# Performance work log

Hardware: AMD Instinct MI355X
Metric: run time of the kernel (lower is better)

The kernel has to match this reference:

```python
import jax, jax.numpy as jnp
import numpy as np

K = 2048          # codes per class
NC = 8            # num_classes
CD = 256          # conv_dims
SP = 4            # latent spatial (28 -> 14 -> 7 -> 4)
D = CD * SP * SP  # 4096 codebook vector dim
N = 512           # RoIs


def _conv(x, W, b, stride, pad):
    y = jax.lax.conv_general_dilated(x, W, (stride, stride), [(pad, pad), (pad, pad)],
                                     dimension_numbers=('NCHW', 'OIHW', 'NCHW'))
    return y + b[None, :, None, None]


def _upsample2_ac(x):
    # bilinear upsample x2 with align_corners=True (torch nn.Upsample semantics)
    n, ch, H, W = x.shape
    Ho, Wo = 2 * H, 2 * W
    ys = jnp.arange(Ho) * (H - 1) / (Ho - 1)
    xs = jnp.arange(Wo) * (W - 1) / (Wo - 1)
    y0 = jnp.floor(ys).astype(jnp.int32); y1 = jnp.minimum(y0 + 1, H - 1)
    x0 = jnp.floor(xs).astype(jnp.int32); x1 = jnp.minimum(x0 + 1, W - 1)
    wy = (ys - y0).astype(x.dtype); wx = (xs - x0).astype(x.dtype)
    r = x[:, :, y0, :] * (1 - wy)[None, None, :, None] + x[:, :, y1, :] * wy[None, None, :, None]
    return r[:, :, :, x0] * (1 - wx)[None, None, None, :] + r[:, :, :, x1] * wx[None, None, None, :]


def setup_inputs() -> dict:
    key = jax.random.key(0)
    ks = jax.random.split(key, 20)
    s = 0.02
    inp = {
        'x': jax.random.normal(ks[0], (N, 1, 28, 28), jnp.float32),
        'We0': jax.random.normal(ks[1], (CD, 1, 3, 3), jnp.float32) * s,
        'be0': jnp.zeros((CD,), jnp.float32),
        'We1': jax.random.normal(ks[2], (CD, CD, 3, 3), jnp.float32) * s,
        'be1': jnp.zeros((CD,), jnp.float32),
        'We2': jax.random.normal(ks[3], (CD, CD, 3, 3), jnp.float32) * s,
        'be2': jnp.zeros((CD,), jnp.float32),
        'E': jax.random.normal(ks[4], (K * NC, D), jnp.float32) * s,
        'Wd0': jax.random.normal(ks[5], (CD, CD, 3, 3), jnp.float32) * s,
        'bd0': jnp.zeros((CD,), jnp.float32),
        'Wd1': jax.random.normal(ks[6], (CD, CD, 3, 3), jnp.float32) * s,
        'bd1': jnp.zeros((CD,), jnp.float32),
        'Wd2': jax.random.normal(ks[7], (CD, CD, 3, 3), jnp.float32) * s,
        'bd2': jnp.zeros((CD,), jnp.float32),
        'Wo': jax.random.normal(ks[8], (1, CD, 3, 3), jnp.float32) * s,
        'bo': jnp.zeros((1,), jnp.float32),
        'c': jax.random.randint(ks[9], (N,), 0, NC, jnp.int32),
    }
    return inp


def reference(x, We0, be0, We1, be1, We2, be2, E, Wd0, bd0, Wd1, bd1, Wd2, bd2, Wo, bo, c):
    # ---- encoder: 3 stride-2 convs, relu on all but the last ----
    h = jax.nn.relu(_conv(x, We0, be0, 2, 1))   # [N,CD,14,14]
    h = jax.nn.relu(_conv(h, We1, be1, 2, 1))   # [N,CD,7,7]
    h = _conv(h, We2, be2, 2, 1)                # [N,CD,4,4]
    z_e = h.reshape(N, D)                       # flattened latent, == z_e_x [N,D,1,1]

    # ---- class-conditional VQ ----
    # torch code loops over unique classes and concatenates -> output is in
    # stable-sorted-by-class order; replicate via stable argsort permutation.
    perm = jnp.argsort(c)  # stable
    # distances to the FULL table, then mask codes outside the sample's class slice
    d2 = (jnp.sum(z_e * z_e, axis=1, keepdims=True)         # [N,1]
          - 2.0 * z_e @ E.T                                  # [N,K*NC]
          + jnp.sum(E * E, axis=1)[None, :])
    code_cls = jnp.arange(K * NC, dtype=c.dtype) // K        # class of each code row
    d2 = jnp.where(code_cls[None, :] == c[:, None], d2, jnp.inf)
    idx = jnp.argmin(d2, axis=1)                             # global code index (includes key*K offset)

    q_det = jax.lax.stop_gradient(E)[idx]                    # vq_st uses detached codebook
    z_q_st = z_e + jax.lax.stop_gradient(q_det - z_e)        # straight-through
    z_q_bar = E[idx]                                         # gradient flows to codebook

    z_q_st_p = z_q_st[perm]
    z_q_bar_p = z_q_bar[perm]

    # ---- decoder: (upsample2 bilinear ac + conv + relu) x3, pad=0 on layer k==num_conv-2 ----
    xd = z_q_st_p.reshape(N, CD, SP, SP)
    xd = jax.nn.relu(_conv(_upsample2_ac(xd), Wd0, bd0, 1, 1))  # 4->8
    xd = jax.nn.relu(_conv(_upsample2_ac(xd), Wd1, bd1, 1, 0))  # 8->16->14
    xd = jax.nn.relu(_conv(_upsample2_ac(xd), Wd2, bd2, 1, 1))  # 14->28
    x_tilde = jax.nn.sigmoid(_conv(xd, Wo, bo, 1, 1))           # [N,1,28,28]

    return (x_tilde, z_e.reshape(N, D, 1, 1), z_q_bar_p.reshape(N, D, 1, 1))
```

## Files before the change

kernel.cpp:

```cpp
#include <hip/hip_runtime.h>
#include <hip/hip_bf16.h>
#include <cstdint>
#include <cstddef>

#define CDIV(a,b) (((a)+(b)-1)/(b))

typedef __attribute__((ext_vector_type(8))) short vbf8;
typedef __attribute__((ext_vector_type(4))) float vf4;

__device__ inline unsigned short f2bf(float f) {
  unsigned u = __float_as_uint(f);
  unsigned r = (u + 0x7fffu + ((u >> 16) & 1u)) >> 16;
  return (unsigned short)r;
}
__device__ inline float bf2f(unsigned short h) { return __uint_as_float(((unsigned)h) << 16); }

__global__ __launch_bounds__(256) void conv_e0_cl_kernel(
    const float* __restrict__ x, const float* __restrict__ W,
    const float* __restrict__ b, unsigned short* __restrict__ hi,
    unsigned short* __restrict__ lo)
{
  __shared__ float s_img[784];
  const int n = blockIdx.x;
  const int co = threadIdx.x;
  for (int i = threadIdx.x; i < 784; i += 256) s_img[i] = x[(size_t)n*784 + i];
  float w[9];
#pragma unroll
  for (int t = 0; t < 9; ++t) w[t] = W[co*9 + t];
  const float bb = b[co];
  __syncthreads();
  for (int p = 0; p < 196; ++p) {
    int y = p / 14, xo = p % 14;
    float a = bb;
#pragma unroll
    for (int t = 0; t < 9; ++t) {
      int yi = 2*y + t/3 - 1, xi = 2*xo + t%3 - 1;
      if (yi >= 0 && yi < 28 && xi >= 0 && xi < 28) a = fmaf(w[t], s_img[yi*28 + xi], a);
    }
    a = fmaxf(a, 0.f);
    unsigned short h = f2bf(a);
    size_t oidx = ((size_t)n*196 + p)*256 + co;
    hi[oidx] = h;
    lo[oidx] = f2bf(a - bf2f(h));
  }
}

__global__ __launch_bounds__(256) void wprep2_kernel(
    const float* __restrict__ W, unsigned short* __restrict__ Whi,
    unsigned short* __restrict__ Wlo)
{
  int idx = blockIdx.x*256 + threadIdx.x;
  if (idx >= 589824) return;
  int j   = idx & 7;
  int co  = (idx >> 3) & 255;
  int cig = (idx >> 11) & 31;
  int t   = idx >> 16;
  int ci  = cig*8 + j;
  float w = W[((size_t)co*256 + ci)*9 + t];
  unsigned short h = f2bf(w);
  Whi[idx] = h;
  Wlo[idx] = f2bf(w - bf2f(h));
}

template<int STRIDE, int HO, int WO, int WOP, int ROWS, int HI, int WI, int PAD,
         int ACT, int SPLIT, int OUTMODE>
__global__ __launch_bounds__(256, 2) void convmfma_kernel(
    const unsigned short* __restrict__ inT, const unsigned short* __restrict__ inTlo,
    const vbf8* __restrict__ Wt, const vbf8* __restrict__ Wtlo,
    const float* __restrict__ bias,
    unsigned short* __restrict__ outT, unsigned short* __restrict__ outTlo,
    float* __restrict__ outF)
{
  constexpr int NFM = ROWS*WOP/16;
  constexpr int RIN = (ROWS-1)*STRIDE + 3;
  constexpr int WS  = (WOP-1)*STRIDE + 3;
  constexpr int NG  = SPLIT ? 12 : 4;
  __shared__ vbf8 sA[RIN*WS*8];

  const int n  = blockIdx.x;
  const int y0 = blockIdx.y * ROWS;
  const int tid = threadIdx.x;
  const int lane = tid & 63;
  const int wv = tid >> 6;
  const int l15 = lane & 15;
  const int lq  = lane >> 4;
  const int cobase = wv * 64;

  int abase[NFM];
#pragma unroll
  for (int mf = 0; mf < NFM; ++mf) {
    int pos = mf*16 + l15;
    abase[mf] = (pos / WOP) * STRIDE * WS + (pos % WOP) * STRIDE;
  }

  vf4 acc[NFM][4];
#pragma unroll
  for (int mf = 0; mf < NFM; ++mf)
#pragma unroll
    for (int nf = 0; nf < 4; ++nf) acc[mf][nf] = (vf4){0.f, 0.f, 0.f, 0.f};

#pragma unroll 1
  for (int g = 0; g < NG; ++g) {
    const int cc = g & 3;
    const unsigned short* src = (SPLIT && g >= 8) ? inTlo : inT;
    const vbf8* wsrc = (SPLIT && g >= 4 && g < 8) ? Wtlo : Wt;
    for (int idx = tid; idx < RIN*WS*8; idx += 256) {
      int lin = idx >> 3, cig = idx & 7;
      int r = lin / WS, x = lin % WS;
      int yi = y0*STRIDE + r - PAD, xi = x - PAD;
      vbf8 v = {0,0,0,0,0,0,0,0};
      if (yi >= 0 && yi < HI && xi >= 0 && xi < WI)
        v = *(const vbf8*)(src + ((((size_t)n*HI + yi)*WI + xi)*256 + cc*64 + cig*8));
      sA[(lin*8 + cig) ^ (lin & 7)] = v;
    }
    __syncthreads();
#pragma unroll
    for (int t = 0; t < 9; ++t) {
      const int dy = t/3, dx = t%3;
#pragma unroll
      for (int kk = 0; kk < 2; ++kk) {
        vbf8 bfr[4];
        const int cig_g = cc*8 + kk*4 + lq;
#pragma unroll
        for (int nf = 0; nf < 4; ++nf)
          bfr[nf] = wsrc[((size_t)t*32 + cig_g)*256 + cobase + nf*16 + l15];
        vbf8 af[NFM];
        const int cigl = kk*4 + lq;
#pragma unroll
        for (int mf = 0; mf < NFM; ++mf) {
          int lin = abase[mf] + dy*WS + dx;
          af[mf] = sA[(lin*8 + cigl) ^ (lin & 7)];
        }
#pragma unroll
        for (int mf = 0; mf < NFM; ++mf)
#pragma unroll
          for (int nf = 0; nf < 4; ++nf)
            acc[mf][nf] = __builtin_amdgcn_mfma_f32_16x16x32_bf16(af[mf], bfr[nf], acc[mf][nf], 0, 0, 0);
      }
    }
    __syncthreads();
  }

  float bb[4];
#pragma unroll
  for (int nf = 0; nf < 4; ++nf) bb[nf] = bias[cobase + nf*16 + l15];
#pragma unroll
  for (int mf = 0; mf < NFM; ++mf) {
#pragma unroll
    for (int q = 0; q < 4; ++q) {
      int pos = mf*16 + lq*4 + q;
      int y = y0 + pos/WOP, x = pos % WOP;
      if (WOP > WO && x >= WO) continue;
      if (HO % ROWS != 0 && y >= HO) continue;
#pragma unroll
      for (int nf = 0; nf < 4; ++nf) {
        float v = acc[mf][nf][q] + bb[nf];
        if (ACT) v = fmaxf(v, 0.f);
        const int co = cobase + nf*16 + l15;
        if (OUTMODE == 2) {
          outF[((size_t)n*256 + co)*(HO*WO) + y*WO + x] = v;
        } else {
          size_t oidx = (((size_t)n*HO + y)*WO + x)*256 + co;
          unsigned short h = f2bf(v);
          outT[oidx] = h;
          if (OUTMODE == 1) outTlo[oidx] = f2bf(v - bf2f(h));
        }
      }
    }
  }
}

template<int H, int W>
__global__ __launch_bounds__(256) void upsample_cl_kernel(
    const unsigned short* __restrict__ in, unsigned short* __restrict__ out, int nimg)
{
  constexpr int Ho = 2*H, Wo = 2*W;
  int idx = blockIdx.x*256 + threadIdx.x;
  int total = nimg * Ho * Wo * 32;
  if (idx >= total) return;
  int cig = idx & 31; int rest = idx >> 5;
  int xo = rest % Wo; rest /= Wo;
  int yo = rest % Ho; int n = rest / Ho;
  float ys = (float)(yo*(H-1)) / (float)(Ho-1);
  float xs = (float)(xo*(W-1)) / (float)(Wo-1);
  int ya = (int)ys; int yb = (ya+1 < H) ? ya+1 : H-1;
  int xa = (int)xs; int xb = (xa+1 < W) ? xa+1 : W-1;
  float wy = ys - (float)ya, wx = xs - (float)xa;
  const unsigned short* base = in + (size_t)n*H*W*256 + cig*8;
  vbf8 vaa = *(const vbf8*)(base + ((size_t)ya*W + xa)*256);
  vbf8 vab = *(const vbf8*)(base + ((size_t)ya*W + xb)*256);
  vbf8 vba = *(const vbf8*)(base + ((size_t)yb*W + xa)*256);
  vbf8 vbb = *(const vbf8*)(base + ((size_t)yb*W + xb)*256);
  vbf8 o;
#pragma unroll
  for (int j = 0; j < 8; ++j) {
    float r0 = bf2f((unsigned short)vaa[j])*(1.f-wy) + bf2f((unsigned short)vba[j])*wy;
    float r1 = bf2f((unsigned short)vab[j])*(1.f-wy) + bf2f((unsigned short)vbb[j])*wy;
    o[j] = (short)f2bf(r0*(1.f-wx) + r1*wx);
  }
  *(vbf8*)(out + (((size_t)n*Ho + yo)*Wo + xo)*256 + cig*8) = o;
}

__global__ __launch_bounds__(256) void conv_out_t_kernel(
    const unsigned short* __restrict__ a2t, const float* __restrict__ Wo,
    const float* __restrict__ bo, float* __restrict__ out)
{
  const int n = blockIdx.x;
  const int y0 = blockIdx.y * 14;
  const int tid = threadIdx.x;
  __shared__ vbf8 s_in[16*30*8];
  __shared__ float s_w[9*64];
  float acc[2] = {0.f, 0.f};
  for (int cc = 0; cc < 4; ++cc) {
    for (int idx = tid; idx < 16*30*8; idx += 256) {
      int lin = idx >> 3, cig = idx & 7;
      int r = lin / 30, xx = lin % 30;
      int yi = y0 + r - 1, xi = xx - 1;
      vbf8 v = {0,0,0,0,0,0,0,0};
      if (yi >= 0 && yi < 28 && xi >= 0 && xi < 28)
        v = *(const vbf8*)(a2t + (((size_t)n*28 + yi)*28 + xi)*256 + cc*64 + cig*8);
      s_in[(lin*8 + cig) ^ (lin & 7)] = v;
    }
    for (int idx = tid; idx < 576; idx += 256) {
      int t = idx / 64, cil = idx % 64;
      s_w[t*64 + cil] = Wo[((size_t)cc*64 + cil)*9 + t];
    }
    __syncthreads();
#pragma unroll
    for (int q = 0; q < 2; ++q) {
      int p = tid + q*256;
      if (p < 392) {
        int y = p / 28, x = p % 28;
        float a = acc[q];
#pragma unroll
        for (int t = 0; t < 9; ++t) {
          int lin = (y + t/3)*30 + (x + t%3);
#pragma unroll
          for (int cig = 0; cig < 8; ++cig) {
            vbf8 v = s_in[(lin*8 + cig) ^ (lin & 7)];
#pragma unroll
            for (int j = 0; j < 8; ++j)
              a = fmaf(bf2f((unsigned short)v[j]), s_w[t*64 + cig*8 + j], a);
          }
        }
        acc[q] = a;
      }
    }
    __syncthreads();
  }
  const float bb = bo[0];
  for (int q = 0; q < 2; ++q) {
    int p = tid + q*256;
    if (p < 392) {
      int y = y0 + p/28, x = p%28;
      out[(size_t)n*784 + y*28 + x] = 1.f/(1.f + expf(-(acc[q] + bb)));
    }
  }
}

__global__ __launch_bounds__(256) void enorm_kernel(
    const float* __restrict__ E, float* __restrict__ norms)
{
  const int k = blockIdx.x;
  const float4* row = (const float4*)(E + (size_t)k*4096);
  float s = 0.f;
  for (int i = threadIdx.x; i < 1024; i += 256) {
    float4 v = row[i];
    s += v.x*v.x + v.y*v.y + v.z*v.z + v.w*v.w;
  }
  __shared__ float red[256];
  red[threadIdx.x] = s; __syncthreads();
  for (int off = 128; off > 0; off >>= 1) {
    if (threadIdx.x < off) red[threadIdx.x] += red[threadIdx.x + off];
    __syncthreads();
  }
  if (threadIdx.x == 0) norms[k] = red[0];
}

__global__ __launch_bounds__(256) void etrans_kernel(
    const float* __restrict__ E, unsigned short* __restrict__ Et)
{
  const int cb = blockIdx.x;
  const int kb = blockIdx.y;
  const int t = threadIdx.x;
  const int cl = t >> 2;
  const int seg = t & 3;
  const int code = cb*64 + cl;
  const int k0 = kb*64 + seg*16;
  const float4* src = (const float4*)(E + (size_t)code*4096 + k0);
  float4 v0 = src[0], v1 = src[1], v2 = src[2], v3 = src[3];
  vbf8 a, b;
  a[0]=(short)f2bf(v0.x); a[1]=(short)f2bf(v0.y); a[2]=(short)f2bf(v0.z); a[3]=(short)f2bf(v0.w);
  a[4]=(short)f2bf(v1.x); a[5]=(short)f2bf(v1.y); a[6]=(short)f2bf(v1.z); a[7]=(short)f2bf(v1.w);
  b[0]=(short)f2bf(v2.x); b[1]=(short)f2bf(v2.y); b[2]=(short)f2bf(v2.z); b[3]=(short)f2bf(v2.w);
  b[4]=(short)f2bf(v3.x); b[5]=(short)f2bf(v3.y); b[6]=(short)f2bf(v3.z); b[7]=(short)f2bf(v3.w);
  vbf8* dst = (vbf8*)Et;
  dst[(size_t)(k0 >> 3)*16384 + code]     = a;
  dst[((size_t)(k0 >> 3) + 1)*16384 + code] = b;
}

__global__ __launch_bounds__(512) void perm_kernel(
    const int* __restrict__ c, int* __restrict__ perm, int* __restrict__ off)
{
  __shared__ int sc[512];
  __shared__ int cnt[8];
  __shared__ int base[9];
  const int i = threadIdx.x;
  sc[i] = c[i];
  if (i < 8) cnt[i] = 0;
  __syncthreads();
  atomicAdd(&cnt[sc[i]], 1);
  __syncthreads();
  if (i == 0) { int a = 0; for (int j = 0; j < 8; ++j) { base[j] = a; a += cnt[j]; } base[8] = a; }
  __syncthreads();
  const int ci = sc[i];
  int rank = 0;
  for (int j = 0; j < i; ++j) rank += (sc[j] == ci) ? 1 : 0;
  perm[base[ci] + rank] = i;
  if (i < 9) off[i] = base[i];
}

__global__ __launch_bounds__(256) void vq_coarse_kernel(
    const float* __restrict__ zE, const vbf8* __restrict__ Etv,
    const float* __restrict__ norms, const int* __restrict__ perm,
    const int* __restrict__ offs, float* __restrict__ dco)
{
  const int cls = blockIdx.x;
  const int mb  = blockIdx.y;
  const int kb  = blockIdx.z;
  const int s0 = offs[cls];
  const int total = offs[cls+1] - s0;
  int nrows = total - mb*64;
  if (nrows <= 0) return;
  if (nrows > 64) nrows = 64;

  __shared__ vbf8 sA[64*8];
  __shared__ int srow_s[64];
  const int tid = threadIdx.x;
  if (tid < 64) srow_s[tid] = (tid < nrows) ? perm[s0 + mb*64 + tid] : -1;
  __syncthreads();

  const int lane = tid & 63;
  const int wv = tid >> 6;
  const int l15 = lane & 15;
  const int lq  = lane >> 4;

  const int myrow = tid >> 2;
  const int seg = tid & 3;
  const int srow_mine = srow_s[myrow];
  const float* zbase = (srow_mine >= 0) ? (zE + (size_t)srow_mine*4096 + seg*16) : nullptr;

  const int cbase = cls*2048 + kb*256 + wv*64;

  vf4 acc[4][4];
#pragma unroll
  for (int mf = 0; mf < 4; ++mf)
#pragma unroll
    for (int nf = 0; nf < 4; ++nf) acc[mf][nf] = (vf4){0.f, 0.f, 0.f, 0.f};

#pragma unroll 1
  for (int k0 = 0; k0 < 4096; k0 += 64) {
    {
      float4 v0, v1, v2, v3;
      if (zbase) {
        const float4* p = (const float4*)(zbase + k0);
        v0 = p[0]; v1 = p[1]; v2 = p[2]; v3 = p[3];
      } else {
        v0 = v1 = v2 = v3 = (float4){0.f, 0.f, 0.f, 0.f};
      }
      vbf8 a, b;
      a[0]=(short)f2bf(v0.x); a[1]=(short)f2bf(v0.y); a[2]=(short)f2bf(v0.z); a[3]=(short)f2bf(v0.w);
      a[4]=(short)f2bf(v1.x); a[5]=(short)f2bf(v1.y); a[6]=(short)f2bf(v1.z); a[7]=(short)f2bf(v1.w);
      b[0]=(short)f2bf(v2.x); b[1]=(short)f2bf(v2.y); b[2]=(short)f2bf(v2.z); b[3]=(short)f2bf(v2.w);
      b[4]=(short)f2bf(v3.x); b[5]=(short)f2bf(v3.y); b[6]=(short)f2bf(v3.z); b[7]=(short)f2bf(v3.w);
      int c0 = seg*2;
      sA[myrow*8 + (c0 ^ (myrow & 7))]       = a;
      sA[myrow*8 + ((c0 + 1) ^ (myrow & 7))] = b;
    }
    __syncthreads();
#pragma unroll
    for (int kb32 = 0; kb32 < 2; ++kb32) {
      vbf8 af[4], bf[4];
#pragma unroll
      for (int mf = 0; mf < 4; ++mf) {
        int row = mf*16 + l15;
        af[mf] = sA[row*8 + ((kb32*4 + lq) ^ (row & 7))];
      }
      const size_t kg = (size_t)((k0 >> 3) + kb32*4 + lq);
#pragma unroll
      for (int nf = 0; nf < 4; ++nf)
        bf[nf] = Etv[kg*16384 + cbase + nf*16 + l15];
#pragma unroll
      for (int mf = 0; mf < 4; ++mf)
#pragma unroll
        for (int nf = 0; nf < 4; ++nf)
          acc[mf][nf] = __builtin_amdgcn_mfma_f32_16x16x32_bf16(af[mf], bf[nf], acc[mf][nf], 0, 0, 0);
    }
    __syncthreads();
  }

  float nrm[4];
#pragma unroll
  for (int nf = 0; nf < 4; ++nf) nrm[nf] = norms[cbase + nf*16 + l15];
#pragma unroll
  for (int mf = 0; mf < 4; ++mf) {
#pragma unroll
    for (int q = 0; q < 4; ++q) {
      int slot = mf*16 + lq*4 + q;
      if (slot < nrows) {
        int s = srow_s[slot];
        float* drow = dco + (size_t)s*2048 + (kb*256 + wv*64);
#pragma unroll
        for (int nf = 0; nf < 4; ++nf)
          drow[nf*16 + l15] = nrm[nf] - 2.f*acc[mf][nf][q];
      }
    }
  }
}

__global__ __launch_bounds__(256) void vq_select_kernel(
    const float* __restrict__ dco, const int* __restrict__ c,
    const float* __restrict__ zE, const float* __restrict__ E,
    int* __restrict__ codes)
{
  const int s = blockIdx.x;
  const int cls = c[s];
  const int tid = threadIdx.x;
  const float* drow = dco + (size_t)s*2048;

  float mn = 3.4e38f, mx = -3.4e38f;
  for (int j = tid; j < 2048; j += 256) {
    float d = drow[j];
    mn = fminf(mn, d); mx = fmaxf(mx, d);
  }
  __shared__ float smn[256], smx[256];
  smn[tid] = mn; smx[tid] = mx;
  __syncthreads();
  for (int o = 128; o > 0; o >>= 1) {
    if (tid < o) { smn[tid] = fminf(smn[tid], smn[tid+o]); smx[tid] = fmaxf(smx[tid], smx[tid+o]); }
    __syncthreads();
  }
  const float dmin = smn[0], dmax = smx[0];
  const float margin = 0.06f*(dmax - dmin) + 1e-6f*fabsf(dmin) + 1e-20f;

  __shared__ int cand[64];
  __shared__ int cnt_s;
  if (tid == 0) cnt_s = 0;
  __syncthreads();
  for (int j = tid; j < 2048; j += 256) {
    if (drow[j] <= dmin + margin) {
      int p = atomicAdd(&cnt_s, 1);
      if (p < 64) cand[p] = j;
    }
  }
  __syncthreads();
  const int cnt = (cnt_s < 64) ? cnt_s : 64;

  __shared__ double red[256];
  __shared__ double bestd_s;
  __shared__ int bestc_s;
  if (tid == 0) { bestd_s = 1.0e300; bestc_s = 0x7fffffff; }
  __syncthreads();
  const float* zrow = zE + (size_t)s*4096;
  for (int t = 0; t < cnt; ++t) {
    const int gcode = cls*2048 + cand[t];
    const float* erow = E + (size_t)gcode*4096;
    double p = 0.0;
    for (int e2 = tid; e2 < 4096; e2 += 256) {
      double ev = (double)erow[e2];
      double zv = (double)zrow[e2];
      p += ev*ev - 2.0*zv*ev;
    }
    red[tid] = p;
    __syncthreads();
    for (int o = 128; o > 0; o >>= 1) {
      if (tid < o) red[tid] += red[tid+o];
      __syncthreads();
    }
    if (tid == 0) {
      double d = red[0];
      if (d < bestd_s || (d == bestd_s && gcode < bestc_s)) { bestd_s = d; bestc_s = gcode; }
    }
    __syncthreads();
  }
  if (tid == 0) codes[s] = bestc_s;
}

__global__ __launch_bounds__(256) void gather_t_kernel(
    const int* __restrict__ codes, const int* __restrict__ perm,
    const float* __restrict__ E, float* __restrict__ zq, unsigned short* __restrict__ zqt)
{
  const int i = blockIdx.x;
  const int s = perm[i];
  const int code = codes[s];
  const float4* src = (const float4*)(E + (size_t)code*4096);
  float4* dst = (float4*)(zq + (size_t)i*4096);
  for (int t = threadIdx.x; t < 1024; t += 256) {
    float4 v = src[t];
    dst[t] = v;
    int e0 = t*4;
    int ci = e0 >> 4, sp = e0 & 15;
    unsigned short* zp = zqt + ((size_t)i*16 + sp)*256 + ci;
    zp[0]   = f2bf(v.x);
    zp[256] = f2bf(v.y);
    zp[512] = f2bf(v.z);
    zp[768] = f2bf(v.w);
  }
}

extern "C" void kernel_launch(void* const* d_in, const int* in_sizes, int n_in,
                              void* d_out, int out_size, void* d_ws, size_t ws_size,
                              hipStream_t stream) {
  const float* x   = (const float*)d_in[0];
  const float* We0 = (const float*)d_in[1];
  const float* be0 = (const float*)d_in[2];
  const float* We1 = (const float*)d_in[3];
  const float* be1 = (const float*)d_in[4];
  const float* We2 = (const float*)d_in[5];
  const float* be2 = (const float*)d_in[6];
  const float* E   = (const float*)d_in[7];
  const float* Wd0 = (const float*)d_in[8];
  const float* bd0 = (const float*)d_in[9];
  const float* Wd1 = (const float*)d_in[10];
  const float* bd1 = (const float*)d_in[11];
  const float* Wd2 = (const float*)d_in[12];
  const float* bd2 = (const float*)d_in[13];
  const float* Wo  = (const float*)d_in[14];
  const float* bo  = (const float*)d_in[15];
  const int*   c   = (const int*)d_in[16];

  float* out = (float*)d_out;
  float* z_e = out + (size_t)512*784;
  float* zq  = z_e + (size_t)512*4096;

  char* ws = (char*)d_ws;
  size_t off = 0;
  float* norms = (float*)(ws + off); off += 65536;
  int* codes = (int*)(ws + off); off += 2048;
  int* perm = (int*)(ws + off); off += 2048;
  int* offs = (int*)(ws + off); off += 256;
  float* dco = (float*)(ws + off); off += (size_t)512*2048*4;
  unsigned short* zqt = (unsigned short*)(ws + off); off += (size_t)512*16*256*2;
  unsigned short* Et = (unsigned short*)(ws + off); off += (size_t)512*16384*8*2;
  unsigned short* Wt0  = (unsigned short*)(ws + off); off += 1179648;
  unsigned short* Wt0l = (unsigned short*)(ws + off); off += 1179648;
  unsigned short* Wt1  = (unsigned short*)(ws + off); off += 1179648;
  unsigned short* Wt1l = (unsigned short*)(ws + off); off += 1179648;
  unsigned short* Wt2  = (unsigned short*)(ws + off); off += 1179648;
  unsigned short* Wt2l = (unsigned short*)(ws + off); off += 1179648;
  unsigned short* We1h = (unsigned short*)(ws + off); off += 1179648;
  unsigned short* We1l = (unsigned short*)(ws + off); off += 1179648;
  unsigned short* We2h = (unsigned short*)(ws + off); off += 1179648;
  unsigned short* We2l = (unsigned short*)(ws + off); off += 1179648;
  char* big = ws + off;
  size_t avail = (ws_size > off) ? ws_size - off : 0;

  int NB = 512;
  while (NB > 1 && (size_t)NB * 1350656ull > avail) NB >>= 1;
  const int nch = 512 / NB;

  size_t o = 0;
  unsigned short* h0h = (unsigned short*)(big + o); o += (size_t)NB*100352;
  unsigned short* h0l = (unsigned short*)(big + o); o += (size_t)NB*100352;
  unsigned short* h1h = (unsigned short*)(big + o); o += (size_t)NB*25088;
  unsigned short* h1l = (unsigned short*)(big + o); o += (size_t)NB*25088;
  unsigned short* u0t = (unsigned short*)(big + o); o += (size_t)NB*32768;
  unsigned short* a0t = (unsigned short*)(big + o); o += (size_t)NB*32768;
  unsigned short* u1t = (unsigned short*)(big + o); o += (size_t)NB*131072;
  unsigned short* a1t = (unsigned short*)(big + o); o += (size_t)NB*100352;
  unsigned short* u2t = (unsigned short*)(big + o); o += (size_t)NB*401408;
  unsigned short* a2t = (unsigned short*)(big + o); o += (size_t)NB*401408;

  wprep2_kernel<<<CDIV(589824,256), 256, 0, stream>>>(Wd0, Wt0, Wt0l);
  wprep2_kernel<<<CDIV(589824,256), 256, 0, stream>>>(Wd1, Wt1, Wt1l);
  wprep2_kernel<<<CDIV(589824,256), 256, 0, stream>>>(Wd2, Wt2, Wt2l);
  wprep2_kernel<<<CDIV(589824,256), 256, 0, stream>>>(We1, We1h, We1l);
  wprep2_kernel<<<CDIV(589824,256), 256, 0, stream>>>(We2, We2h, We2l);
  enorm_kernel<<<16384, 256, 0, stream>>>(E, norms);
  etrans_kernel<<<dim3(256,64), 256, 0, stream>>>(E, Et);

  for (int ch = 0; ch < nch; ++ch) {
    conv_e0_cl_kernel<<<NB, 256, 0, stream>>>(x + (size_t)ch*NB*784, We0, be0, h0h, h0l);
    convmfma_kernel<2,7,7,8,2, 14,14,1,1,1,1><<<dim3(NB,4), 256, 0, stream>>>(
        h0h, h0l, (const vbf8*)We1h, (const vbf8*)We1l, be1, h1h, h1l, nullptr);
    convmfma_kernel<2,4,4,4,4, 7,7,1,0,1,2><<<dim3(NB,1), 256, 0, stream>>>(
        h1h, h1l, (const vbf8*)We2h, (const vbf8*)We2l, be2, nullptr, nullptr,
        z_e + (size_t)ch*NB*4096);
  }
  perm_kernel<<<1, 512, 0, stream>>>(c, perm, offs);
  vq_coarse_kernel<<<dim3(8,8,8), 256, 0, stream>>>(
      z_e, (const vbf8*)Et, norms, perm, offs, dco);
  vq_select_kernel<<<512, 256, 0, stream>>>(dco, c, z_e, E, codes);
  gather_t_kernel<<<512, 256, 0, stream>>>(codes, perm, E, zq, zqt);

  for (int ch = 0; ch < nch; ++ch) {
    const unsigned short* zt = zqt + (size_t)ch*NB*16*256;
    upsample_cl_kernel<4,4><<<CDIV(NB*2048,256), 256, 0, stream>>>(zt, u0t, NB);
    convmfma_kernel<1,8,8,8,8, 8,8,1,1,0,0><<<dim3(NB,1), 256, 0, stream>>>(
        u0t, nullptr, (const vbf8*)Wt0, nullptr, bd0, a0t, nullptr, nullptr);
    upsample_cl_kernel<8,8><<<CDIV(NB*8192,256), 256, 0, stream>>>(a0t, u1t, NB);
    convmfma_kernel<1,14,14,16,4, 16,16,0,1,0,0><<<dim3(NB,4), 256, 0, stream>>>(
        u1t, nullptr, (const vbf8*)Wt1, nullptr, bd1, a1t, nullptr, nullptr);
    upsample_cl_kernel<14,14><<<CDIV(NB*25088,256), 256, 0, stream>>>(a1t, u2t, NB);
    convmfma_kernel<1,28,28,28,4, 28,28,1,1,0,0><<<dim3(NB,7), 256, 0, stream>>>(
        u2t, nullptr, (const vbf8*)Wt2, nullptr, bd2, a2t, nullptr, nullptr);
    conv_out_t_kernel<<<dim3(NB,2), 256, 0, stream>>>(a2t, Wo, bo, out + (size_t)ch*NB*784);
  }
}
```

Measured before the change: 1.920 ms.

## Reuse staged split-precision inputs across hi/lo weights and shrink conv register tiles

In the split-precision encoder convs, the hi input tile is now staged once and used with both the hi and lo weights, cutting the stage loop from 12 passes to 8. The launch bound is raised from 2 to 3 blocks per SM and several per-block tiles are shrunk: fewer rows for the 8x8 conv and a column offset that splits the 28-wide conv into 16- and 12-column launches. Smaller tiles lower accumulator register pressure so more blocks can be resident. The cost is more blocks, extra halo reloads and one extra kernel launch per chunk for the last decoder conv.

Result: slower. 2.663 ms (+38.7%).

```diff
diff --git a/kernel.cpp b/kernel.cpp
--- a/kernel.cpp
+++ b/kernel.cpp
@@ -62,9 +62,9 @@
   Wlo[idx] = f2bf(w - bf2f(h));
 }
 
-template<int STRIDE, int HO, int WO, int WOP, int ROWS, int HI, int WI, int PAD,
-         int ACT, int SPLIT, int OUTMODE>
-__global__ __launch_bounds__(256, 2) void convmfma_kernel(
+template<int STRIDE, int HO, int WO, int X0, int WOP, int ROWS, int HI, int WI,
+         int PAD, int ACT, int SPLIT, int OUTMODE>
+__global__ __launch_bounds__(256, 3) void convmfma_kernel(
     const unsigned short* __restrict__ inT, const unsigned short* __restrict__ inTlo,
     const vbf8* __restrict__ Wt, const vbf8* __restrict__ Wtlo,
     const float* __restrict__ bias,
@@ -74,7 +74,7 @@
   constexpr int NFM = ROWS*WOP/16;
   constexpr int RIN = (ROWS-1)*STRIDE + 3;
   constexpr int WS  = (WOP-1)*STRIDE + 3;
-  constexpr int NG  = SPLIT ? 12 : 4;
+  constexpr int NSTG = SPLIT ? 8 : 4;
   __shared__ vbf8 sA[RIN*WS*8];
 
   const int n  = blockIdx.x;
@@ -100,42 +100,46 @@
     for (int nf = 0; nf < 4; ++nf) acc[mf][nf] = (vf4){0.f, 0.f, 0.f, 0.f};
 
 #pragma unroll 1
-  for (int g = 0; g < NG; ++g) {
+  for (int g = 0; g < NSTG; ++g) {
     const int cc = g & 3;
-    const unsigned short* src = (SPLIT && g >= 8) ? inTlo : inT;
-    const vbf8* wsrc = (SPLIT && g >= 4 && g < 8) ? Wtlo : Wt;
+    const unsigned short* src = (SPLIT && g >= 4) ? inTlo : inT;
     for (int idx = tid; idx < RIN*WS*8; idx += 256) {
       int lin = idx >> 3, cig = idx & 7;
       int r = lin / WS, x = lin % WS;
-      int yi = y0*STRIDE + r - PAD, xi = x - PAD;
+      int yi = y0*STRIDE + r - PAD, xi = X0*STRIDE + x - PAD;
       vbf8 v = {0,0,0,0,0,0,0,0};
       if (yi >= 0 && yi < HI && xi >= 0 && xi < WI)
         v = *(const vbf8*)(src + ((((size_t)n*HI + yi)*WI + xi)*256 + cc*64 + cig*8));
       sA[(lin*8 + cig) ^ (lin & 7)] = v;
     }
     __syncthreads();
-#pragma unroll
-    for (int t = 0; t < 9; ++t) {
-      const int dy = t/3, dx = t%3;
-#pragma unroll
-      for (int kk = 0; kk < 2; ++kk) {
-        vbf8 bfr[4];
-        const int cig_g = cc*8 + kk*4 + lq;
-#pragma unroll
-        for (int nf = 0; nf < 4; ++nf)
-          bfr[nf] = wsrc[((size_t)t*32 + cig_g)*256 + cobase + nf*16 + l15];
-        vbf8 af[NFM];
-        const int cigl = kk*4 + lq;
-#pragma unroll
-        for (int mf = 0; mf < NFM; ++mf) {
-          int lin = abase[mf] + dy*WS + dx;
-          af[mf] = sA[(lin*8 + cigl) ^ (lin & 7)];
+    const int nw = (SPLIT && g < 4) ? 2 : 1;
+#pragma unroll 1
+    for (int w = 0; w < nw; ++w) {
+      const vbf8* wsrc = (SPLIT && g < 4 && w == 1) ? Wtlo : Wt;
+#pragma unroll
+      for (int t = 0; t < 9; ++t) {
+        const int dy = t/3, dx = t%3;
+#pragma unroll
+        for (int kk = 0; kk < 2; ++kk) {
+          vbf8 bfr[4];
+          const int cig_g = cc*8 + kk*4 + lq;
+#pragma unroll
+          for (int nf = 0; nf < 4; ++nf)
+            bfr[nf] = wsrc[((size_t)t*32 + cig_g)*256 + cobase + nf*16 + l15];
+          vbf8 af[NFM];
+          const int cigl = kk*4 + lq;
+#pragma unroll
+          for (int mf = 0; mf < NFM; ++mf) {
+            int lin = abase[mf] + dy*WS + dx;
+            af[mf] = sA[(lin*8 + cigl) ^ (lin & 7)];
+          }
+#pragma unroll
+          for (int mf = 0; mf < NFM; ++mf)
+#pragma unroll
+            for (int nf = 0; nf < 4; ++nf)
+              acc[mf][nf] = __builtin_amdgcn_mfma_f32_16x16x32_bf16(af[mf], bfr[nf], acc[mf][nf], 0, 0, 0);
         }
-#pragma unroll
-        for (int mf = 0; mf < NFM; ++mf)
-#pragma unroll
-          for (int nf = 0; nf < 4; ++nf)
-            acc[mf][nf] = __builtin_amdgcn_mfma_f32_16x16x32_bf16(af[mf], bfr[nf], acc[mf][nf], 0, 0, 0);
       }
     }
     __syncthreads();
@@ -149,8 +153,8 @@
 #pragma unroll
     for (int q = 0; q < 4; ++q) {
       int pos = mf*16 + lq*4 + q;
-      int y = y0 + pos/WOP, x = pos % WOP;
-      if (WOP > WO && x >= WO) continue;
+      int y = y0 + pos/WOP, x = X0 + pos % WOP;
+      if (X0 + WOP > WO && x >= WO) continue;
       if (HO % ROWS != 0 && y >= HO) continue;
 #pragma unroll
       for (int nf = 0; nf < 4; ++nf) {
@@ -581,9 +585,9 @@
 
   for (int ch = 0; ch < nch; ++ch) {
     conv_e0_cl_kernel<<<NB, 256, 0, stream>>>(x + (size_t)ch*NB*784, We0, be0, h0h, h0l);
-    convmfma_kernel<2,7,7,8,2, 14,14,1,1,1,1><<<dim3(NB,4), 256, 0, stream>>>(
+    convmfma_kernel<2,7,7,0,8,4, 14,14,1,1,1,1><<<dim3(NB,2), 256, 0, stream>>>(
         h0h, h0l, (const vbf8*)We1h, (const vbf8*)We1l, be1, h1h, h1l, nullptr);
-    convmfma_kernel<2,4,4,4,4, 7,7,1,0,1,2><<<dim3(NB,1), 256, 0, stream>>>(
+    convmfma_kernel<2,4,4,0,4,4, 7,7,1,0,1,2><<<dim3(NB,1), 256, 0, stream>>>(
         h1h, h1l, (const vbf8*)We2h, (const vbf8*)We2l, be2, nullptr, nullptr,
         z_e + (size_t)ch*NB*4096);
   }
@@ -596,13 +600,15 @@
   for (int ch = 0; ch < nch; ++ch) {
     const unsigned short* zt = zqt + (size_t)ch*NB*16*256;
     upsample_cl_kernel<4,4><<<CDIV(NB*2048,256), 256, 0, stream>>>(zt, u0t, NB);
-    convmfma_kernel<1,8,8,8,8, 8,8,1,1,0,0><<<dim3(NB,1), 256, 0, stream>>>(
+    convmfma_kernel<1,8,8,0,8,4, 8,8,1,1,0,0><<<dim3(NB,2), 256, 0, stream>>>(
         u0t, nullptr, (const vbf8*)Wt0, nullptr, bd0, a0t, nullptr, nullptr);
     upsample_cl_kernel<8,8><<<CDIV(NB*8192,256), 256, 0, stream>>>(a0t, u1t, NB);
-    convmfma_kernel<1,14,14,16,4, 16,16,0,1,0,0><<<dim3(NB,4), 256, 0, stream>>>(
+    convmfma_kernel<1,14,14,0,16,4, 16,16,0,1,0,0><<<dim3(NB,4), 256, 0, stream>>>(
         u1t, nullptr, (const vbf8*)Wt1, nullptr, bd1, a1t, nullptr, nullptr);
     upsample_cl_kernel<14,14><<<CDIV(NB*25088,256), 256, 0, stream>>>(a1t, u2t, NB);
-    convmfma_kernel<1,28,28,28,4, 28,28,1,1,0,0><<<dim3(NB,7), 256, 0, stream>>>(
+    convmfma_kernel<1,28,28,0,16,4, 28,28,1,1,0,0><<<dim3(NB,7), 256, 0, stream>>>(
+        u2t, nullptr, (const vbf8*)Wt2, nullptr, bd2, a2t, nullptr, nullptr);
+    convmfma_kernel<1,28,28,16,12,4, 28,28,1,1,0,0><<<dim3(NB,7), 256, 0, stream>>>(
         u2t, nullptr, (const vbf8*)Wt2, nullptr, bd2, a2t, nullptr, nullptr);
     conv_out_t_kernel<<<dim3(NB,2), 256, 0, stream>>>(a2t, Wo, bo, out + (size_t)ch*NB*784);
   }
```
